# Performance work log

Measured on AMD Instinct MI355X. Metric: run time of the kernel, lower is better.

Reference implementation:

```python
import jax, jax.numpy as jnp
import numpy as np

G, N_REAL, C_IN, C_EDGE, H, D, C_EOUT = 4096, 31, 64, 64, 4, 64, 64
N_NODE = N_REAL + 1  # 32, last local node is the supernode


def setup_inputs() -> dict:
    key = jax.random.key(0)
    # per-graph edge template: bidirectional ring over real nodes (consecutive (u,v),(v,u) pairs),
    # then edges (u, supernode)
    u = np.arange(N_REAL)
    v = (u + 1) % N_REAL
    ring_src = np.stack([u, v], 1).reshape(-1)
    ring_dst = np.stack([v, u], 1).reshape(-1)
    ls = np.concatenate([ring_src, np.arange(N_REAL)])
    ld = np.concatenate([ring_dst, np.full(N_REAL, N_REAL)])
    Eg = ls.shape[0]  # 93
    off = np.arange(G) * N_NODE
    edge_index = np.stack([(off[:, None] + ls[None, :]).reshape(-1),
                           (off[:, None] + ld[None, :]).reshape(-1)])
    N = G * N_NODE
    E = G * Eg
    k1, k2, k3, k4, k5 = jax.random.split(key, 5)
    return {
        "x": jax.random.normal(k1, (N, C_IN), jnp.float32),
        "edge_index": jnp.asarray(edge_index, jnp.int32),
        "edge_inform": jax.random.normal(k2, (E, C_EDGE), jnp.float32) * 0.1,
        "batch": jnp.asarray(np.repeat(np.arange(G), N_NODE), jnp.int32),
        "edge_num": jnp.asarray(np.full(G, Eg), jnp.int32),
        "W_lin_l": jax.random.normal(k3, (C_IN + C_EDGE, H * D), jnp.float32) * 0.05,
        "att_l": jax.random.normal(k4, (1, H, D), jnp.float32) * 0.1,
        "bias": jnp.zeros((D,), jnp.float32),
        "W_ec": jax.random.normal(k5, (C_EDGE, C_EOUT), jnp.float32) * 0.1,
        "b_ec": jnp.zeros((C_EOUT,), jnp.float32),
    }


def reference(x, edge_index, edge_inform, batch, edge_num, W_lin_l, att_l, bias, W_ec, b_ec):
    # graph structure is static metadata -> numpy
    ei = np.asarray(edge_index)
    en = np.asarray(edge_num)
    N = x.shape[0]
    G_ = en.shape[0]
    Eg = int(en[0])
    n = N // G_
    src = jnp.asarray(ei[0])
    dst = jnp.asarray(ei[1])
    Hh, Dd = att_l.shape[1], att_l.shape[2]

    # degree counting (the per-edge python loop in the original)
    deg = jnp.zeros((N,), x.dtype).at[dst].add(1.0)

    # GAT-style edge attention + scatter-sum
    h = jnp.concatenate([x[src], edge_inform], axis=1) @ W_lin_l  # [E, H*D]
    h = h.reshape(-1, Hh, Dd)
    alpha = jax.nn.leaky_relu(jnp.sum(h * att_l, axis=-1))  # [E,H], slope 0.01
    amax = jax.ops.segment_max(alpha, dst, num_segments=N)
    ex = jnp.exp(alpha - amax[dst])
    a = ex / (jax.ops.segment_sum(ex, dst, num_segments=N)[dst] + 1e-16)
    xi = jax.ops.segment_sum(h * a[..., None], dst, num_segments=N)  # [N,H,D]
    out = xi.mean(axis=1) + bias

    # per-graph edge aggregation (structure uniform across graphs by construction)
    le = ei.reshape(2, G_, Eg) - (np.arange(G_) * n)[None, :, None]
    l0, l1 = le[0, 0], le[1, 0]  # local template indices, same for every graph
    midx = np.nonzero((l1 != n - 1) & (l0 != l1))[0]  # mask: drop supernode-dst & self-loops
    even = midx[0::2]
    C = edge_inform.shape[1]
    inf_g = edge_inform.reshape(G_, Eg, C)

    mdst = jnp.asarray(l1[midx])
    eisum = jax.vmap(lambda v: jax.ops.segment_sum(v, mdst, num_segments=n - 1))(inf_g[:, midx])  # [G,n-1,C]

    es, ed = l0[even], l1[even]
    deg_g = deg.reshape(G_, n)
    norm = deg_g[:, es] + deg_g[:, ed] - 2.0  # edge_norm; divide by edge_norm - 1
    temp = (eisum[:, es] + eisum[:, ed] - inf_g[:, even]) / (norm - 1.0)[..., None]  # [G,P,C]
    temps2 = jnp.repeat(temp, 2, axis=1)  # each temp appended twice

    l1_all = jnp.asarray(l1)
    cnt = jnp.zeros((n,), x.dtype).at[l1_all].add(1.0)
    esum_all = jax.vmap(lambda v: jax.ops.segment_sum(v, l1_all, num_segments=n))(inf_g)
    emean = esum_all / cnt[None, :, None]  # scatter reduce='mean'

    gather = jnp.concatenate([temps2, emean, emean[:, : n - 1]], axis=1).reshape(-1, C)
    new_edge_inform = jax.nn.leaky_relu(gather @ W_ec + b_ec)
    return out, new_edge_inform
```

## Files before the change

### kernel.cpp

```cpp
#include <hip/hip_runtime.h>
#include <hip/hip_fp16.h>

#define NUM_G 4096
#define OUT2_OFF ((size_t)NUM_G * 32 * 64)

typedef _Float16 half8  __attribute__((ext_vector_type(8)));
typedef _Float16 half4v __attribute__((ext_vector_type(4)));
typedef float    floatx4 __attribute__((ext_vector_type(4)));

__device__ __forceinline__ float lrelu(float v) { return v > 0.f ? v : 0.01f * v; }

__device__ __forceinline__ int swz(int row, int col) {
    return row * 64 + (col ^ ((row & 7) << 3));
}

__global__ void setup_prep(const float* __restrict__ W, const float* __restrict__ att,
                           const float* __restrict__ Wec,
                           _Float16* __restrict__ vp16, _Float16* __restrict__ BT,
                           _Float16* __restrict__ BT2)
{
    const int t = threadIdx.x, b = blockIdx.x;
    if (b < 16) {
        __shared__ _Float16 T[8][256];
        const int kbase = b * 8;
        #pragma unroll
        for (int rr = 0; rr < 8; ++rr)
            T[rr][t] = (_Float16)W[(kbase + rr) * 256 + t];
        __syncthreads();
        const int d = t >> 2, h = t & 3;
        half8 v;
        #pragma unroll
        for (int kk = 0; kk < 8; ++kk) v[kk] = T[kk][h * 64 + d];
        *(half8*)(BT + d * 512 + h * 128 + kbase) = v;
    } else if (b == 16) {
        for (int i = t; i < 1024; i += 256) {
            const int h8 = i >> 6, k = i & 63;
            float acc = 0.f;
            if (h8 < 8) {
                const int h = h8 & 3, ro = (h8 < 4) ? 0 : 64;
                const float4* wr = (const float4*)(W + (ro + k) * 256 + h * 64);
                const float4* ar = (const float4*)(att + h * 64);
                #pragma unroll
                for (int d4 = 0; d4 < 16; ++d4) {
                    float4 wv = wr[d4], av = ar[d4];
                    acc += wv.x * av.x + wv.y * av.y + wv.z * av.z + wv.w * av.w;
                }
            }
            vp16[i] = (_Float16)acc;
        }
    } else {
        __shared__ _Float16 T2[64][65];
        #pragma unroll
        for (int j = 0; j < 16; ++j) {
            const int idx = j * 256 + t;
            T2[idx >> 6][idx & 63] = (_Float16)Wec[idx];
        }
        __syncthreads();
        #pragma unroll
        for (int j = 0; j < 16; ++j) {
            const int idx = j * 256 + t;
            BT2[idx] = T2[idx & 63][idx >> 6];
        }
    }
}

__global__ __launch_bounds__(256, 2) void fused_main(
    const float* __restrict__ x, const float* __restrict__ einf,
    const float* __restrict__ bias, const float* __restrict__ bec,
    const _Float16* __restrict__ vp16, const _Float16* __restrict__ BT,
    const _Float16* __restrict__ BT2,
    float* __restrict__ out, float* __restrict__ out2)
{
    __shared__ __align__(16) _Float16 R[2][128 * 64];
    __shared__ __align__(16) _Float16 A2[2][64 * 64];
    __shared__ __align__(16) float    sal[2][128 * 9];
    __shared__ __align__(16) _Float16 al4h[2][96 * 4];
    __shared__ __align__(16) _Float16 virt[2][512];

    const int t = threadIdx.x;
    const int g0 = blockIdx.x * 2;
    const int lane = t & 63;
    const int w = t >> 6;
    const int m16 = lane & 15, q = lane >> 4;

    #pragma unroll
    for (int gi = 0; gi < 2; ++gi) {
        const float4* xg4 = (const float4*)(x + (size_t)(g0 + gi) * 2048);
        for (int i = t; i < 512; i += 256) {
            float4 v = xg4[i];
            half4v h4 = {(_Float16)v.x, (_Float16)v.y, (_Float16)v.z, (_Float16)v.w};
            *(half4v*)(R[gi] + swz(i >> 4, (i & 15) * 4)) = h4;
        }
        const float4* eg4 = (const float4*)(einf + (size_t)(g0 + gi) * 5952);
        for (int i = t; i < 1488; i += 256) {
            float4 v = eg4[i];
            half4v h4 = {(_Float16)v.x, (_Float16)v.y, (_Float16)v.z, (_Float16)v.w};
            *(half4v*)(R[gi] + swz(32 + (i >> 4), (i & 15) * 4)) = h4;
        }
        if (t < 24) {
            half8 z = {0, 0, 0, 0, 0, 0, 0, 0};
            *(half8*)(R[gi] + 125 * 64 + t * 8) = z;
        }
    }
    half8 bF0 = *(const half8*)(vp16 + m16 * 64 + q * 8);
    half8 bF1 = *(const half8*)(vp16 + m16 * 64 + 32 + q * 8);
    __syncthreads();

    #pragma unroll
    for (int gi = 0; gi < 2; ++gi) {
        #pragma unroll
        for (int j = 0; j < 2; ++j) {
            const int tile = w * 2 + j;
            const int row = tile * 16 + m16;
            half8 aF0 = *(const half8*)(R[gi] + swz(row, q * 8));
            half8 aF1 = *(const half8*)(R[gi] + swz(row, 32 + q * 8));
            floatx4 s = {0.f, 0.f, 0.f, 0.f};
            s = __builtin_amdgcn_mfma_f32_16x16x32_f16(aF0, bF0, s, 0, 0, 0);
            s = __builtin_amdgcn_mfma_f32_16x16x32_f16(aF1, bF1, s, 0, 0, 0);
            if (m16 < 8) {
                #pragma unroll
                for (int r = 0; r < 4; ++r)
                    sal[gi][(tile * 16 + q * 4 + r) * 9 + m16] = s[r];
            }
        }
    }
    __syncthreads();

    if (w < 2) {
        const int gi = w;
        const int i = lane;
        const bool act = (i < 31);
        float av[4], mx[4], wv[4];
        #pragma unroll
        for (int h = 0; h < 4; ++h)
            av[h] = act ? lrelu(sal[gi][i * 9 + h] + sal[gi][(94 + i) * 9 + 4 + h]) : -1e30f;
        #pragma unroll
        for (int h = 0; h < 4; ++h) {
            float m = av[h];
            #pragma unroll
            for (int off = 32; off > 0; off >>= 1)
                m = fmaxf(m, __shfl_xor(m, off, 64));
            mx[h] = m;
        }
        #pragma unroll
        for (int h = 0; h < 4; ++h) {
            float e = act ? __expf(av[h] - mx[h]) : 0.f;
            float s = e;
            #pragma unroll
            for (int off = 32; off > 0; off >>= 1)
                s += __shfl_xor(s, off, 64);
            wv[h] = e / (s + 1e-16f);
        }
        if (act) {
            half4v hv = {(_Float16)wv[0], (_Float16)wv[1], (_Float16)wv[2], (_Float16)wv[3]};
            *(half4v*)(al4h[gi] + (62 + i) * 4) = hv;
        }
        asm volatile("s_waitcnt lgkmcnt(0)" ::: "memory");
        __builtin_amdgcn_wave_barrier();
        half8 aV;
        #pragma unroll
        for (int j = 0; j < 8; ++j) {
            const int e = q * 8 + j;
            aV[j] = (m16 < 4 && e < 31) ? al4h[gi][(62 + e) * 4 + m16] : (_Float16)0.f;
        }
        #pragma unroll
        for (int hf = 0; hf < 2; ++hf) {
            const int base = hf ? 94 : 0;
            #pragma unroll
            for (int nt = 0; nt < 4; ++nt) {
                half8 bV;
                #pragma unroll
                for (int j = 0; j < 8; ++j) {
                    const int e = q * 8 + j;
                    bV[j] = (e < 31) ? R[gi][swz(base + e, nt * 16 + m16)] : (_Float16)0.f;
                }
                floatx4 vc = {0.f, 0.f, 0.f, 0.f};
                vc = __builtin_amdgcn_mfma_f32_16x16x32_f16(aV, bV, vc, 0, 0, 0);
                if (q == 0) {
                    #pragma unroll
                    for (int r = 0; r < 4; ++r)
                        virt[gi][r * 128 + hf * 64 + nt * 16 + m16] = (_Float16)vc[r];
                }
            }
        }
    } else {
        const int gi = w - 2;
        #pragma unroll
        for (int rep = 0; rep < 2; ++rep) {
            const int item = lane * 2 + rep;
            if (item < 124) {
                const int n = item >> 2, h = item & 3;
                const int s1 = (n + 30) % 31, s2 = (n + 1) % 31;
                const int e1 = 2 * s1, e2 = 2 * n + 1;
                const float a1 = lrelu(sal[gi][s1 * 9 + h] + sal[gi][(32 + e1) * 9 + 4 + h]);
                const float a2 = lrelu(sal[gi][s2 * 9 + h] + sal[gi][(32 + e2) * 9 + 4 + h]);
                const float m = fmaxf(a1, a2);
                const float x1 = __expf(a1 - m), x2 = __expf(a2 - m);
                const float inv = 1.f / (x1 + x2 + 1e-16f);
                al4h[gi][e1 * 4 + h] = (_Float16)(x1 * inv);
                al4h[gi][e2 * 4 + h] = (_Float16)(x2 * inv);
            }
        }
        for (int idx = lane; idx < 992; idx += 64) {
            const int r = idx >> 4, c = (idx & 15) * 4;
            half4v v;
            if (r < 31) {
                const int ra = 2 * ((r + 30) % 31), rb = 2 * r + 1, rc = 2 * ((r + 1) % 31) + 1;
                v = *(const half4v*)(R[gi] + swz(32 + ra, c)) + *(const half4v*)(R[gi] + swz(32 + rb, c))
                  + *(const half4v*)(R[gi] + swz(32 + rc, c));
            } else {
                const int jj = r - 31;
                const int ra = 2 * ((jj + 30) % 31), rb = 2 * jj + 1;
                v = (*(const half4v*)(R[gi] + swz(32 + ra, c)) + *(const half4v*)(R[gi] + swz(32 + rb, c)))
                    * (_Float16)0.5f;
            }
            *(half4v*)(A2[gi] + swz(r, c)) = v;
        }
        {
            const int c = lane;
            float s = 0.f;
            for (int i = 0; i < 31; ++i) s += (float)R[gi][swz(94 + i, c)];
            A2[gi][swz(62, c)] = (_Float16)(s * (1.f / 31.f));
            A2[gi][swz(63, c)] = (_Float16)0.f;
        }
    }
    __syncthreads();

    const int co = w * 16 + m16;
    half8 b2a = *(const half8*)(BT2 + co * 64 + q * 8);
    half8 b2b = *(const half8*)(BT2 + co * 64 + 32 + q * 8);

    {
        const int n1c = (16 + m16 < 31) ? 16 + m16 : 30;
        const int s1_0 = (m16 + 30) % 31, s2_0 = (m16 + 1) % 31;
        const int e1_0 = 2 * s1_0, e2_0 = 2 * m16 + 1;
        const int s1_1 = (n1c + 30) % 31, s2_1 = (n1c + 1) % 31;
        const int e1_1 = 2 * s1_1, e2_1 = 2 * n1c + 1;
        half4v a1_0[2], a2_0[2], a1_1[2], a2_1[2];
        #pragma unroll
        for (int gi = 0; gi < 2; ++gi) {
            a1_0[gi] = *(const half4v*)(al4h[gi] + e1_0 * 4);
            a2_0[gi] = *(const half4v*)(al4h[gi] + e2_0 * 4);
            a1_1[gi] = *(const half4v*)(al4h[gi] + e1_1 * 4);
            a2_1[gi] = *(const half4v*)(al4h[gi] + e2_1 * 4);
        }
        floatx4 z = {0.f, 0.f, 0.f, 0.f};
        floatx4 acc0[2] = {z, z}, acc1[2] = {z, z};
        #pragma unroll
        for (int hf = 0; hf < 2; ++hf) {
            const int rA0 = hf ? 32 + e1_0 : s1_0, rB0 = hf ? 32 + e2_0 : s2_0;
            const int rA1 = hf ? 32 + e1_1 : s1_1, rB1 = hf ? 32 + e2_1 : s2_1;
            #pragma unroll
            for (int kc = 0; kc < 2; ++kc) {
                const int k0 = kc * 32 + q * 8;
                half8 x1[2], x2[2], y1[2], y2[2];
                #pragma unroll
                for (int gi = 0; gi < 2; ++gi) {
                    x1[gi] = *(const half8*)(R[gi] + swz(rA0, k0));
                    x2[gi] = *(const half8*)(R[gi] + swz(rB0, k0));
                    y1[gi] = *(const half8*)(R[gi] + swz(rA1, k0));
                    y2[gi] = *(const half8*)(R[gi] + swz(rB1, k0));
                }
                #pragma unroll
                for (int h = 0; h < 4; ++h) {
                    half8 b = *(const half8*)(BT + co * 512 + h * 128 + hf * 64 + k0);
                    #pragma unroll
                    for (int gi = 0; gi < 2; ++gi) {
                        half8 af0 = x1[gi] * a1_0[gi][h] + x2[gi] * a2_0[gi][h];
                        acc0[gi] = __builtin_amdgcn_mfma_f32_16x16x32_f16(af0, b, acc0[gi], 0, 0, 0);
                        half8 af1 = y1[gi] * a1_1[gi][h] + y2[gi] * a2_1[gi][h];
                        half8 vv = *(const half8*)(virt[gi] + h * 128 + hf * 64 + k0);
                        af1 = (m16 == 15) ? vv : af1;
                        acc1[gi] = __builtin_amdgcn_mfma_f32_16x16x32_f16(af1, b, acc1[gi], 0, 0, 0);
                    }
                }
            }
        }
        const float bv = bias[co];
        #pragma unroll
        for (int gi = 0; gi < 2; ++gi) {
            float* og = out + (size_t)(g0 + gi) * 2048;
            #pragma unroll
            for (int r = 0; r < 4; ++r) {
                og[(q * 4 + r) * 64 + co]        = 0.25f * acc0[gi][r] + bv;
                og[(16 + q * 4 + r) * 64 + co]   = 0.25f * acc1[gi][r] + bv;
            }
        }
    }

    {
        floatx4 z = {0.f, 0.f, 0.f, 0.f};
        floatx4 acc2[2][4];
        #pragma unroll
        for (int gi = 0; gi < 2; ++gi)
            #pragma unroll
            for (int mt = 0; mt < 4; ++mt) acc2[gi][mt] = z;
        #pragma unroll
        for (int kk = 0; kk < 2; ++kk) {
            half8 b = kk ? b2b : b2a;
            #pragma unroll
            for (int gi = 0; gi < 2; ++gi) {
                #pragma unroll
                for (int mt = 0; mt < 4; ++mt) {
                    half8 a = *(const half8*)(A2[gi] + swz(mt * 16 + m16, kk * 32 + q * 8));
                    acc2[gi][mt] = __builtin_amdgcn_mfma_f32_16x16x32_f16(a, b, acc2[gi][mt], 0, 0, 0);
                }
            }
        }
        const float bv2 = bec[co];
        #pragma unroll
        for (int gi = 0; gi < 2; ++gi) {
            float* o2 = out2 + (size_t)(g0 + gi) * 8000;
            #pragma unroll
            for (int mt = 0; mt < 4; ++mt) {
                #pragma unroll
                for (int r = 0; r < 4; ++r) {
                    const int row = mt * 16 + q * 4 + r;
                    if (row >= 63) continue;
                    const float v = lrelu(acc2[gi][mt][r] + bv2);
                    if (row < 31) {
                        o2[(2 * row) * 64 + co]     = v;
                        o2[(2 * row + 1) * 64 + co] = v;
                    } else if (row < 62) {
                        o2[(62 + row - 31) * 64 + co] = v;
                        o2[(94 + row - 31) * 64 + co] = v;
                    } else {
                        o2[93 * 64 + co] = v;
                    }
                }
            }
        }
    }
}

extern "C" void kernel_launch(void* const* d_in, const int* in_sizes, int n_in,
                              void* d_out, int out_size, void* d_ws, size_t ws_size,
                              hipStream_t stream) {
    const float* x    = (const float*)d_in[0];
    const float* einf = (const float*)d_in[2];
    const float* W    = (const float*)d_in[5];
    const float* att  = (const float*)d_in[6];
    const float* bias = (const float*)d_in[7];
    const float* Wec  = (const float*)d_in[8];
    const float* bec  = (const float*)d_in[9];
    float* out  = (float*)d_out;
    float* out2 = out + OUT2_OFF;

    _Float16* vp16 = (_Float16*)d_ws;
    _Float16* BT   = (_Float16*)((char*)d_ws + 2048);
    _Float16* BT2  = (_Float16*)((char*)d_ws + 2048 + 65536);

    setup_prep<<<18, 256, 0, stream>>>(W, att, Wec, vp16, BT, BT2);
    fused_main<<<NUM_G / 2, 256, 0, stream>>>(x, einf, bias, bec, vp16, BT, BT2, out, out2);
}
```

Before: 326.3 us.

## Build edge-conv MFMA operands directly from R, drop A2 buffer, raise occupancy

The separate pass that gathered and summed edge rows into a shared A2 buffer is removed. The MFMA A operands are now formed on the fly by adding three swizzled rows of R and scaling. The edge-mean row goes into R row 127, and rows 125/126 are assumed to be zero padding. Dropping A2 frees 16 KB of LDS per block, so launch bounds move to 3 blocks per CU for more occupancy, at the cost of more LDS reads and half-precision adds in the MFMA loop, plus register pressure under the tighter bound.

```diff
diff --git a/kernel.cpp b/kernel.cpp
--- a/kernel.cpp
+++ b/kernel.cpp
@@ -64,7 +64,7 @@
     }
 }
 
-__global__ __launch_bounds__(256, 2) void fused_main(
+__global__ __launch_bounds__(256, 3) void fused_main(
     const float* __restrict__ x, const float* __restrict__ einf,
     const float* __restrict__ bias, const float* __restrict__ bec,
     const _Float16* __restrict__ vp16, const _Float16* __restrict__ BT,
@@ -72,7 +72,6 @@
     float* __restrict__ out, float* __restrict__ out2)
 {
     __shared__ __align__(16) _Float16 R[2][128 * 64];
-    __shared__ __align__(16) _Float16 A2[2][64 * 64];
     __shared__ __align__(16) float    sal[2][128 * 9];
     __shared__ __align__(16) _Float16 al4h[2][96 * 4];
     __shared__ __align__(16) _Float16 virt[2][512];
@@ -201,27 +200,11 @@
                 al4h[gi][e2 * 4 + h] = (_Float16)(x2 * inv);
             }
         }
-        for (int idx = lane; idx < 992; idx += 64) {
-            const int r = idx >> 4, c = (idx & 15) * 4;
-            half4v v;
-            if (r < 31) {
-                const int ra = 2 * ((r + 30) % 31), rb = 2 * r + 1, rc = 2 * ((r + 1) % 31) + 1;
-                v = *(const half4v*)(R[gi] + swz(32 + ra, c)) + *(const half4v*)(R[gi] + swz(32 + rb, c))
-                  + *(const half4v*)(R[gi] + swz(32 + rc, c));
-            } else {
-                const int jj = r - 31;
-                const int ra = 2 * ((jj + 30) % 31), rb = 2 * jj + 1;
-                v = (*(const half4v*)(R[gi] + swz(32 + ra, c)) + *(const half4v*)(R[gi] + swz(32 + rb, c)))
-                    * (_Float16)0.5f;
-            }
-            *(half4v*)(A2[gi] + swz(r, c)) = v;
-        }
         {
             const int c = lane;
             float s = 0.f;
             for (int i = 0; i < 31; ++i) s += (float)R[gi][swz(94 + i, c)];
-            A2[gi][swz(62, c)] = (_Float16)(s * (1.f / 31.f));
-            A2[gi][swz(63, c)] = (_Float16)0.f;
+            R[gi][swz(127, c)] = (_Float16)(s * (1.f / 31.f));
         }
     }
     __syncthreads();
@@ -296,13 +279,40 @@
             #pragma unroll
             for (int mt = 0; mt < 4; ++mt) acc2[gi][mt] = z;
         #pragma unroll
-        for (int kk = 0; kk < 2; ++kk) {
-            half8 b = kk ? b2b : b2a;
-            #pragma unroll
-            for (int gi = 0; gi < 2; ++gi) {
-                #pragma unroll
-                for (int mt = 0; mt < 4; ++mt) {
-                    half8 a = *(const half8*)(A2[gi] + swz(mt * 16 + m16, kk * 32 + q * 8));
+        for (int mt = 0; mt < 4; ++mt) {
+            const int r_ = mt * 16 + m16;
+            int i1, i2, i3;
+            _Float16 sc;
+            if (r_ < 31) {
+                const int prev = (r_ == 0) ? 30 : r_ - 1;
+                const int next = (r_ == 30) ? 0 : r_ + 1;
+                i1 = 32 + 2 * prev;
+                i2 = 32 + 2 * r_ + 1;
+                i3 = 32 + 2 * next + 1;
+                sc = (_Float16)1.f;
+            } else if (r_ < 62) {
+                const int jj = r_ - 31;
+                const int prevj = (jj == 0) ? 30 : jj - 1;
+                i1 = 32 + 2 * prevj;
+                i2 = 32 + 2 * jj + 1;
+                i3 = 125;
+                sc = (_Float16)0.5f;
+            } else if (r_ == 62) {
+                i1 = 127; i2 = 125; i3 = 126;
+                sc = (_Float16)1.f;
+            } else {
+                i1 = 125; i2 = 126; i3 = 125;
+                sc = (_Float16)1.f;
+            }
+            #pragma unroll
+            for (int kk = 0; kk < 2; ++kk) {
+                const int k0 = kk * 32 + q * 8;
+                half8 b = kk ? b2b : b2a;
+                #pragma unroll
+                for (int gi = 0; gi < 2; ++gi) {
+                    half8 a = (*(const half8*)(R[gi] + swz(i1, k0))
+                             + *(const half8*)(R[gi] + swz(i2, k0))
+                             + *(const half8*)(R[gi] + swz(i3, k0))) * sc;
                     acc2[gi][mt] = __builtin_amdgcn_mfma_f32_16x16x32_f16(a, b, acc2[gi][mt], 0, 0, 0);
                 }
             }
```

Result: faster. 315.6 us (-3.3%).
